# Kernel tuning notes

Hardware: AMD Instinct MI355X
Metric: run time of the kernel (lower is better)

## Reference

```python
import jax, jax.numpy as jnp
import numpy as np

B, S, D_DIM = 32, 512, 1024

def setup_inputs() -> dict:
    key = jax.random.key(0)
    k1, k2, k3, k4 = jax.random.split(key, 4)
    return {
        "D": jax.random.normal(k1, (B, S, D_DIM), dtype=jnp.float32),
        "H": jax.random.normal(k2, (B, S, D_DIM), dtype=jnp.float32),
        # learned params: U is (d+1, d) (xavier-style scale), W is (2d+1,)
        # (original inits W to zeros; we use small random values so the linear
        #  term is exercised — same math either way)
        "U": jax.random.normal(k3, (D_DIM + 1, D_DIM), dtype=jnp.float32) * 0.02,
        "W": jax.random.normal(k4, (2 * D_DIM + 1,), dtype=jnp.float32) * 0.02,
    }

def reference(D, H, U, W):
    # D, H: [B, S, d]; U: [d+1, d]; W: [2d+1]
    d = H.shape[-1]
    ones = jnp.ones(D.shape[:2] + (1,), dtype=D.dtype)
    Daug = jnp.concatenate([D, ones], axis=-1)              # [B, S, d+1]
    # bilinear term: v.U.u  -> [B, Sx, Sy]
    bil = jnp.einsum('bxi,ij,byj->bxy', Daug, U, H)
    # linear term W . concat(D_aug, H): algebraically split — avoids the
    # O(B*S*S*2d) concatenated intermediate of the original implementation
    lin = (Daug @ W[:d + 1])[:, :, None] + (H @ W[d + 1:])[:, None, :]
    return bil + lin
```

## Files before the change

kernel.cpp:

```cpp
#include <hip/hip_runtime.h>


#define D_DIM 1024
#define ROWS 16384

typedef float floatx4 __attribute__((ext_vector_type(4)));
typedef __bf16 bf16x8 __attribute__((ext_vector_type(8)));
typedef __bf16 bf16x4 __attribute__((ext_vector_type(4)));

__device__ inline unsigned short f2bf(float f) {
  unsigned int u = __builtin_bit_cast(unsigned int, f);
  u = (u + 0x7FFFu + ((u >> 16) & 1u)) >> 16;
  return (unsigned short)u;
}

__device__ inline void async_load16(const void* g, void* l) {
  __builtin_amdgcn_global_load_lds(
      (const __attribute__((address_space(1))) void*)g,
      (__attribute__((address_space(3))) void*)l, 16, 0, 0);
}

__global__ __launch_bounds__(256) void transU_kernel(
    const float* __restrict__ U, const float* __restrict__ W,
    unsigned short* __restrict__ Ut, float* __restrict__ Wh) {
  if (blockIdx.x == 0 && blockIdx.y == 0) {
    #pragma unroll
    for (int i = 0; i < 4; ++i)
      Wh[threadIdx.x + 256 * i] = W[D_DIM + 1 + threadIdx.x + 256 * i];
  }
  __shared__ float tile[32][33];
  int n0 = blockIdx.x * 32;
  int k0 = blockIdx.y * 32;
  int t = threadIdx.x;
  int tr = t >> 5, tc = t & 31;
  #pragma unroll
  for (int i = 0; i < 32; i += 8)
    tile[tr + i][tc] = U[(size_t)(k0 + tr + i) * D_DIM + n0 + tc];
  __syncthreads();
  #pragma unroll
  for (int i = 0; i < 32; i += 8)
    Ut[(size_t)(n0 + tr + i) * D_DIM + k0 + tc] = f2bf(tile[tc][tr + i]);
}

template <bool F32_IS_A>
__device__ inline void gemm_core_mixed(
    const unsigned short* __restrict__ Ga,
    const float* __restrict__ Gf,
    const float* __restrict__ Wv,
    bool do_lin, float (&part)[8],
    unsigned short* As, unsigned short* Bs,
    floatx4 (&acc)[4][4]) {
  const int K = D_DIM;
  int tid = threadIdx.x;
  int l = tid & 63, wave = tid >> 6;
  int quad = l >> 4, lrow = l & 15;
  int wm = wave >> 1, wn = wave & 1;

  unsigned short* Sasync = F32_IS_A ? Bs : As;
  unsigned short* Sf32   = F32_IS_A ? As : Bs;

  int srow = 8 * wave + (l >> 3);
  int sq = (l & 7) ^ (l >> 3);
  const unsigned short* gasync = Ga + (size_t)srow * K + sq * 8;

  int rl = lrow & 7, gofs = lrow >> 3;
  int baseA = wm * 512 + gofs * 64 + rl * 8;
  int baseB = wn * 512 + gofs * 64 + rl * 8;

  int qi = tid & 15;
  const float* gf = Gf + (size_t)(tid >> 4) * K + qi * 4;

  for (int k0 = 0; k0 < K; k0 += 64) {
    __syncthreads();
    #pragma unroll
    for (int j = 0; j < 4; ++j)
      async_load16(gasync + (size_t)(32 * j) * K + k0, Sasync + (j * 256 + tid) * 8);
    float4 v[8];
    #pragma unroll
    for (int i = 0; i < 8; ++i)
      v[i] = *(const float4*)(gf + (size_t)(16 * i) * K + k0);
    float4 wq;
    if (do_lin) wq = *(const float4*)(Wv + k0 + qi * 4);
    #pragma unroll
    for (int i = 0; i < 8; ++i) {
      if (do_lin)
        part[i] += v[i].x * wq.x + v[i].y * wq.y + v[i].z * wq.z + v[i].w * wq.w;
      int row = 16 * i + (tid >> 4);
      int q = qi >> 1, half = qi & 1;
      int c = (row >> 3) * 64 + (row & 7) * 8 + (q ^ (row & 7));
      bf16x4 o = { (__bf16)v[i].x, (__bf16)v[i].y, (__bf16)v[i].z, (__bf16)v[i].w };
      *(bf16x4*)(Sf32 + c * 8 + half * 4) = o;
    }
    __syncthreads();
    #pragma unroll
    for (int s = 0; s < 2; ++s) {
      int xq = (s * 4 + quad) ^ rl;
      bf16x8 a[4], b[4];
      #pragma unroll
      for (int mt = 0; mt < 4; ++mt)
        a[mt] = *(const bf16x8*)(As + (baseA + mt * 128 + xq) * 8);
      #pragma unroll
      for (int nt = 0; nt < 4; ++nt)
        b[nt] = *(const bf16x8*)(Bs + (baseB + nt * 128 + xq) * 8);
      #pragma unroll
      for (int mt = 0; mt < 4; ++mt)
        #pragma unroll
        for (int nt = 0; nt < 4; ++nt)
          acc[mt][nt] = __builtin_amdgcn_mfma_f32_16x16x32_bf16(
              a[mt], b[nt], acc[mt][nt], 0, 0, 0);
    }
  }
}

__global__ __launch_bounds__(256) void gemm1_kernel(
    const float* __restrict__ Df,
    const unsigned short* __restrict__ Ut,
    const float* __restrict__ Ubias,
    const float* __restrict__ W,
    unsigned short* __restrict__ T,
    float* __restrict__ linD) {
  __shared__ __align__(16) unsigned short As[128 * 64];
  __shared__ __align__(16) unsigned short Bs[128 * 64];
  int m0 = blockIdx.x * 128, n0 = blockIdx.y * 128;
  int tid = threadIdx.x;
  int lane = tid & 63, wave = tid >> 6;
  int quad = lane >> 4, lrow = lane & 15;
  int wm = wave >> 1, wn = wave & 1;
  bool do_lin = (blockIdx.y == 0);

  float part[8] = {};
  floatx4 acc[4][4] = {};
  gemm_core_mixed<true>(Ut + (size_t)n0 * D_DIM, Df + (size_t)m0 * D_DIM,
                        W, do_lin, part, As, Bs, acc);

  #pragma unroll
  for (int mt = 0; mt < 4; ++mt)
    #pragma unroll
    for (int nt = 0; nt < 4; ++nt) {
      int row = m0 + wm * 64 + mt * 16 + quad * 4;
      int col = n0 + wn * 64 + nt * 16 + lrow;
      float bias = Ubias[col];
      #pragma unroll
      for (int rr = 0; rr < 4; ++rr)
        T[(size_t)(row + rr) * D_DIM + col] = f2bf(acc[mt][nt][rr] + bias);
    }

  if (do_lin) {
    __syncthreads();
    float* red = (float*)As;
    #pragma unroll
    for (int i = 0; i < 8; ++i)
      red[(16 * i + (tid >> 4)) * 16 + (tid & 15)] = part[i];
    __syncthreads();
    if (tid < 128) {
      float s = 0.f;
      #pragma unroll
      for (int j = 0; j < 16; ++j) s += red[tid * 16 + j];
      linD[m0 + tid] = s + W[D_DIM];
    }
  }
}

__global__ __launch_bounds__(256) void gemm2_kernel(
    const unsigned short* __restrict__ Tg,
    const float* __restrict__ Hf,
    const float* __restrict__ Wh,
    const float* __restrict__ linD,
    float* __restrict__ out) {
  __shared__ __align__(16) unsigned short As[128 * 64];
  __shared__ __align__(16) unsigned short Bs[128 * 64];
  __shared__ float linh_s[128];
  int b = blockIdx.x;
  int t = blockIdx.y;
  int m0 = (t >> 2) * 128, n0 = (t & 3) * 128;
  int tid = threadIdx.x;
  int lane = tid & 63, wave = tid >> 6;
  int quad = lane >> 4, lrow = lane & 15;
  int wm = wave >> 1, wn = wave & 1;

  float part[8] = {};
  floatx4 acc[4][4] = {};
  gemm_core_mixed<false>(Tg + ((size_t)b * 512 + m0) * D_DIM,
                         Hf + ((size_t)b * 512 + n0) * D_DIM,
                         Wh, true, part, As, Bs, acc);

  __syncthreads();
  float* red = (float*)Bs;
  #pragma unroll
  for (int i = 0; i < 8; ++i)
    red[(16 * i + (tid >> 4)) * 16 + (tid & 15)] = part[i];
  __syncthreads();
  if (tid < 128) {
    float s = 0.f;
    #pragma unroll
    for (int j = 0; j < 16; ++j) s += red[tid * 16 + j];
    linh_s[tid] = s;
  }
  __syncthreads();

  #pragma unroll
  for (int mt = 0; mt < 4; ++mt)
    #pragma unroll
    for (int nt = 0; nt < 4; ++nt) {
      int row = m0 + wm * 64 + mt * 16 + quad * 4;
      int col = n0 + wn * 64 + nt * 16 + lrow;
      float lh = linh_s[wn * 64 + nt * 16 + lrow];
      #pragma unroll
      for (int rr = 0; rr < 4; ++rr) {
        float v = acc[mt][nt][rr] + linD[b * 512 + row + rr] + lh;
        out[((size_t)b * 512 + row + rr) * 512 + col] = v;
      }
    }
}

extern "C" void kernel_launch(void* const* d_in, const int* in_sizes, int n_in,
                              void* d_out, int out_size, void* d_ws, size_t ws_size,
                              hipStream_t stream) {
  const float* D = (const float*)d_in[0];
  const float* H = (const float*)d_in[1];
  const float* U = (const float*)d_in[2];
  const float* W = (const float*)d_in[3];
  float* out = (float*)d_out;

  char* ws = (char*)d_ws;
  unsigned short* Tbf = (unsigned short*)ws; ws += (size_t)ROWS * D_DIM * 2;
  unsigned short* Ut  = (unsigned short*)ws; ws += (size_t)D_DIM * D_DIM * 2;
  float* linD = (float*)ws;                  ws += (size_t)ROWS * 4;
  float* Wh   = (float*)ws;                  ws += (size_t)D_DIM * 4;

  transU_kernel<<<dim3(32, 32), 256, 0, stream>>>(U, W, Ut, Wh);
  gemm1_kernel<<<dim3(128, 8), 256, 0, stream>>>(D, Ut, U + (size_t)D_DIM * D_DIM, W, Tbf, linD);
  gemm2_kernel<<<dim3(32, 16), 256, 0, stream>>>(Tbf, H, Wh, linD, out);
}
```

Measured before the change: 226.3 us.

## Register-prefetch next fp32 tile and stage W vector in LDS

The GEMM main loop now prefetches the next K-slice of the fp32 operand into registers while the current slice is converted to bf16 and consumed, so global load latency overlaps with MFMA work. The W linear-term vector is copied into LDS once per block instead of being read from global memory every iteration. Swizzled LDS offsets are precomputed, and __syncthreads is replaced by raw barriers with an explicit partial vmcnt wait so the prefetch loads stay in flight. This doubles the fp32 register staging, which may raise register pressure and lower occupancy, and the hand-written waitcnt depends on the exact count of outstanding loads.

```diff
diff --git a/kernel.cpp b/kernel.cpp
--- a/kernel.cpp
+++ b/kernel.cpp
@@ -46,8 +46,8 @@
 __device__ inline void gemm_core_mixed(
     const unsigned short* __restrict__ Ga,
     const float* __restrict__ Gf,
-    const float* __restrict__ Wv,
-    bool do_lin, float (&part)[8],
+    bool do_lin, const float* WvS,
+    float (&part)[8],
     unsigned short* As, unsigned short* Bs,
     floatx4 (&acc)[4][4]) {
   const int K = D_DIM;
@@ -67,31 +67,48 @@
   int baseA = wm * 512 + gofs * 64 + rl * 8;
   int baseB = wn * 512 + gofs * 64 + rl * 8;
 
-  int qi = tid & 15;
-  const float* gf = Gf + (size_t)(tid >> 4) * K + qi * 4;
+  int qi = tid & 15, frow = tid >> 4;
+  const float* gf = Gf + (size_t)frow * K + qi * 4;
+  int half = qi & 1, q = qi >> 1;
+  int cofs[8];
+  #pragma unroll
+  for (int i = 0; i < 8; ++i) {
+    int row = 16 * i + frow;
+    cofs[i] = ((row >> 3) * 64 + (row & 7) * 8 + (q ^ (row & 7))) * 8 + half * 4;
+  }
+
+  float4 vc[8], vn[8];
+  #pragma unroll
+  for (int i = 0; i < 8; ++i)
+    vc[i] = *(const float4*)(gf + (size_t)(16 * i) * K);
 
   for (int k0 = 0; k0 < K; k0 += 64) {
-    __syncthreads();
+    asm volatile("" ::: "memory");
+    __builtin_amdgcn_s_barrier();
+    asm volatile("" ::: "memory");
     #pragma unroll
     for (int j = 0; j < 4; ++j)
       async_load16(gasync + (size_t)(32 * j) * K + k0, Sasync + (j * 256 + tid) * 8);
-    float4 v[8];
+    __builtin_amdgcn_sched_barrier(0);
+    int kn = (k0 + 64 < K) ? (k0 + 64) : k0;
     #pragma unroll
     for (int i = 0; i < 8; ++i)
-      v[i] = *(const float4*)(gf + (size_t)(16 * i) * K + k0);
-    float4 wq;
-    if (do_lin) wq = *(const float4*)(Wv + k0 + qi * 4);
+      vn[i] = *(const float4*)(gf + (size_t)(16 * i) * K + kn);
+    if (do_lin) {
+      float4 wq = *(const float4*)&WvS[k0 + qi * 4];
+      #pragma unroll
+      for (int i = 0; i < 8; ++i)
+        part[i] += vc[i].x * wq.x + vc[i].y * wq.y + vc[i].z * wq.z + vc[i].w * wq.w;
+    }
     #pragma unroll
     for (int i = 0; i < 8; ++i) {
-      if (do_lin)
-        part[i] += v[i].x * wq.x + v[i].y * wq.y + v[i].z * wq.z + v[i].w * wq.w;
-      int row = 16 * i + (tid >> 4);
-      int q = qi >> 1, half = qi & 1;
-      int c = (row >> 3) * 64 + (row & 7) * 8 + (q ^ (row & 7));
-      bf16x4 o = { (__bf16)v[i].x, (__bf16)v[i].y, (__bf16)v[i].z, (__bf16)v[i].w };
-      *(bf16x4*)(Sf32 + c * 8 + half * 4) = o;
-    }
-    __syncthreads();
+      bf16x4 o = { (__bf16)vc[i].x, (__bf16)vc[i].y, (__bf16)vc[i].z, (__bf16)vc[i].w };
+      *(bf16x4*)(Sf32 + cofs[i]) = o;
+    }
+    asm volatile("s_waitcnt vmcnt(8) lgkmcnt(0)" ::: "memory");
+    __builtin_amdgcn_sched_barrier(0);
+    __builtin_amdgcn_s_barrier();
+    asm volatile("" ::: "memory");
     #pragma unroll
     for (int s = 0; s < 2; ++s) {
       int xq = (s * 4 + quad) ^ rl;
@@ -109,7 +126,12 @@
           acc[mt][nt] = __builtin_amdgcn_mfma_f32_16x16x32_bf16(
               a[mt], b[nt], acc[mt][nt], 0, 0, 0);
     }
-  }
+    #pragma unroll
+    for (int i = 0; i < 8; ++i) vc[i] = vn[i];
+  }
+  #pragma unroll
+  for (int i = 0; i < 8; ++i)
+    asm volatile("" :: "v"(vc[i].x));
 }
 
 __global__ __launch_bounds__(256) void gemm1_kernel(
@@ -121,6 +143,7 @@
     float* __restrict__ linD) {
   __shared__ __align__(16) unsigned short As[128 * 64];
   __shared__ __align__(16) unsigned short Bs[128 * 64];
+  __shared__ float WvS[1024];
   int m0 = blockIdx.x * 128, n0 = blockIdx.y * 128;
   int tid = threadIdx.x;
   int lane = tid & 63, wave = tid >> 6;
@@ -128,10 +151,13 @@
   int wm = wave >> 1, wn = wave & 1;
   bool do_lin = (blockIdx.y == 0);
 
+  ((float4*)WvS)[tid] = ((const float4*)W)[tid];
+  __syncthreads();
+
   float part[8] = {};
   floatx4 acc[4][4] = {};
   gemm_core_mixed<true>(Ut + (size_t)n0 * D_DIM, Df + (size_t)m0 * D_DIM,
-                        W, do_lin, part, As, Bs, acc);
+                        do_lin, WvS, part, As, Bs, acc);
 
   #pragma unroll
   for (int mt = 0; mt < 4; ++mt)
@@ -169,6 +195,7 @@
     float* __restrict__ out) {
   __shared__ __align__(16) unsigned short As[128 * 64];
   __shared__ __align__(16) unsigned short Bs[128 * 64];
+  __shared__ float WvS[1024];
   __shared__ float linh_s[128];
   int b = blockIdx.x;
   int t = blockIdx.y;
@@ -178,11 +205,14 @@
   int quad = lane >> 4, lrow = lane & 15;
   int wm = wave >> 1, wn = wave & 1;
 
+  ((float4*)WvS)[tid] = ((const float4*)Wh)[tid];
+  __syncthreads();
+
   float part[8] = {};
   floatx4 acc[4][4] = {};
   gemm_core_mixed<false>(Tg + ((size_t)b * 512 + m0) * D_DIM,
                          Hf + ((size_t)b * 512 + n0) * D_DIM,
-                         Wh, true, part, As, Bs, acc);
+                         true, WvS, part, As, Bs, acc);
 
   __syncthreads();
   float* red = (float*)Bs;
```

Result: no change. 224.1 us (-1.0%).
